# Kernel tuning notes

Hardware: AMD Instinct MI355X
Metric: run time of the kernel (lower is better)

The kernel has to match this reference:

```python
import jax, jax.numpy as jnp
import numpy as np

N_WIRES = 4
DIM = 16  # 2**4 state-vector length; wire 0 = most significant bit


def _ry(state, theta, wire):
    """Apply RY(theta) on `wire`. state: (N,16) real; theta: (N,) or scalar."""
    s = jnp.moveaxis(state.reshape(-1, 2, 2, 2, 2), 1 + wire, 1)
    c = jnp.cos(theta * 0.5)
    sn = jnp.sin(theta * 0.5)
    if jnp.ndim(theta):
        c = c.reshape(-1, 1, 1, 1)
        sn = sn.reshape(-1, 1, 1, 1)
    s0, s1 = s[:, 0], s[:, 1]
    out = jnp.stack([c * s0 - sn * s1, sn * s0 + c * s1], axis=1)
    return jnp.moveaxis(out, 1, 1 + wire).reshape(-1, DIM)


def _cx_perm(control, target):
    idx = np.arange(DIM)
    cbit = (idx >> (N_WIRES - 1 - control)) & 1
    return np.where(cbit == 1, idx ^ (1 << (N_WIRES - 1 - target)), idx)

# Pauli-Z expectation signs per wire: (16, 4)
_Z_SIGNS = np.stack(
    [1.0 - 2.0 * ((np.arange(DIM) >> (N_WIRES - 1 - w)) & 1) for w in range(N_WIRES)],
    axis=1,
).astype(np.float32)
_CX01 = _cx_perm(0, 1); _CX12 = _cx_perm(1, 2); _CX23 = _cx_perm(2, 3)
_CX02 = _cx_perm(0, 2); _CX13 = _cx_perm(1, 3)


def _init_state(n, dtype):
    return jnp.zeros((n, DIM), dtype).at[:, 0].set(1.0)  # |0000>


def _encode(angles):
    """Fresh device + RY(angle_w) on each wire. angles: (N,4) -> state (N,16)."""
    state = _init_state(angles.shape[0], angles.dtype)
    for w in range(N_WIRES):
        state = _ry(state, angles[:, w], w)
    return state


def _measure_z(state):
    return (state * state) @ jnp.asarray(_Z_SIGNS, state.dtype)  # (N,4)


def _quanv_features(angles, rl_params):
    """Encoder + fixed 8-op 'random layer' (5 RY + 3 CX) + MeasureAll(Z)."""
    s = _encode(angles)
    s = _ry(s, rl_params[0], 0)
    s = _ry(s, rl_params[1], 1)
    s = s[:, _CX02]
    s = _ry(s, rl_params[2], 2)
    s = _ry(s, rl_params[3], 3)
    s = s[:, _CX13]
    s = _ry(s, rl_params[4], 0)
    s = s[:, _CX23]
    return _measure_z(s)  # (N,4)


def _attn_raw(angles):
    """Encoder + CX(0,1),CX(1,2),CX(2,3), measure Z on wire 0."""
    s = _encode(angles)
    s = s[:, _CX01]
    s = s[:, _CX12]
    s = s[:, _CX23]
    return _measure_z(s)[:, 0]  # (N,)


def setup_inputs() -> dict:
    key = jax.random.key(0)
    k1, k2, k3 = jax.random.split(key, 3)
    B = 4096
    x = jax.random.uniform(k1, (B, 784), dtype=jnp.float32)
    rl_params = jax.random.normal(k2, (5,), dtype=jnp.float32)
    W = jax.random.normal(k3, (10, 784), dtype=jnp.float32) * 0.03
    b = jnp.zeros((10,), jnp.float32)
    return {"x": x, "rl_params": rl_params, "W": W, "b": b}


def reference(x, rl_params, W, b):
    B = x.shape[0]
    img = x.reshape(B, 28, 28)
    # 2x2 patches in row-major order -> (B*196, 4) with order [tl, tr, bl, br]
    angles = img.reshape(B, 14, 2, 14, 2).transpose(0, 1, 3, 2, 4).reshape(B * 196, 4)
    feats = _quanv_features(angles, rl_params).reshape(B, 196, 4)
    raw = _attn_raw(feats.reshape(B * 196, 4)).reshape(B, 196)
    attn = jax.nn.softmax(raw, axis=1)
    weighted = (feats * attn[:, :, None]).reshape(B, 4 * 14 * 14)
    logits = weighted @ W.T + b
    return jax.nn.log_softmax(logits, axis=-1)
```

## Files before the change

kernel.cpp:

```cpp
#include <hip/hip_runtime.h>

#define NPATCH 196


__device__ __forceinline__ float dot4(float4 a, float4 b) {
    return a.x * b.x + a.y * b.y + a.z * b.z + a.w * b.w;
}

__device__ __forceinline__ float wave_sum_bcast(float x) {
#define DPP_STEP(ctrl, rmask)                                                   \
    x += __int_as_float(__builtin_amdgcn_update_dpp(                            \
        0, __float_as_int(x), (ctrl), (rmask), 0xf, true));
    DPP_STEP(0x111, 0xf)
    DPP_STEP(0x112, 0xf)
    DPP_STEP(0x114, 0xf)
    DPP_STEP(0x118, 0xf)
    DPP_STEP(0x142, 0xa)
    DPP_STEP(0x143, 0xc)
#undef DPP_STEP
    return __int_as_float(__builtin_amdgcn_readlane(__float_as_int(x), 63));
}

__global__ __launch_bounds__(256) void quanv_fused(
    const float* __restrict__ x, const float* __restrict__ rl,
    const float* __restrict__ W, const float* __restrict__ bias,
    float* __restrict__ out)
{
    const int lane = threadIdx.x & 63;
    const int wave = threadIdx.x >> 6;
    const int img  = blockIdx.x * 4 + wave;

    const float* __restrict__ xb = x + (size_t)img * 784;

    float srl2, crl2, srl4, crl4;
    __sincosf(rl[2], &srl2, &crl2);
    __sincosf(rl[4], &srl4, &crl4);
    const float rl0 = rl[0], rl1 = rl[1], rl3v = rl[3];

    auto pairf = [&](int q, float4& fA, float4& fB, float& eA, float& eB) {
        const int r = (2 * q) / 14;
        const int c = (2 * q) - r * 14;
        const float4 top = *reinterpret_cast<const float4*>(xb + 56 * r + 2 * c);
        const float4 bot = *reinterpret_cast<const float4*>(xb + 56 * r + 2 * c + 28);
        {
            float sa, ca; __sincosf(top.x + rl0, &sa, &ca);
            float s2, c2; __sincosf(bot.x, &s2, &c2);
            const float f1 = __cosf(top.y + rl1);
            const float cd = __cosf(bot.y + rl3v);
            const float f0 = crl4 * ca - srl4 * sa * s2;
            const float f2 = crl2 * ca * c2 - srl2 * s2;
            fA = make_float4(f0, f1, f2, f1 * cd * f2);
            eA = __expf(__cosf(f0));
        }
        {
            float sa, ca; __sincosf(top.z + rl0, &sa, &ca);
            float s2, c2; __sincosf(bot.z, &s2, &c2);
            const float f1 = __cosf(top.w + rl1);
            const float cd = __cosf(bot.w + rl3v);
            const float f0 = crl4 * ca - srl4 * sa * s2;
            const float f2 = crl2 * ca * c2 - srl2 * s2;
            fB = make_float4(f0, f1, f2, f1 * cd * f2);
            eB = __expf(__cosf(f0));
        }
    };

    const bool has2 = (lane < 34);
    const int q2 = has2 ? (lane + 64) : lane;

    float4 fA0, fB0, fA1, fB1;
    float eA0, eB0, eA1, eB1;
    pairf(lane, fA0, fB0, eA0, eB0);
    pairf(q2,   fA1, fB1, eA1, eB1);
    if (!has2) { eA1 = 0.f; eB1 = 0.f; }

    const float inv = 1.0f / wave_sum_bcast(eA0 + eB0 + eA1 + eB1);

    const float wA0 = eA0 * inv, wB0 = eB0 * inv;
    const float wA1 = eA1 * inv, wB1 = eB1 * inv;
    const float4 gA0 = make_float4(fA0.x * wA0, fA0.y * wA0, fA0.z * wA0, fA0.w * wA0);
    const float4 gB0 = make_float4(fB0.x * wB0, fB0.y * wB0, fB0.z * wB0, fB0.w * wB0);
    const float4 gA1 = make_float4(fA1.x * wA1, fA1.y * wA1, fA1.z * wA1, fA1.w * wA1);
    const float4 gB1 = make_float4(fB1.x * wB1, fB1.y * wB1, fB1.z * wB1, fB1.w * wB1);

    const float4* __restrict__ W4 = reinterpret_cast<const float4*>(W);
    float acc[10];
    #pragma unroll
    for (int k = 0; k < 10; ++k) {
        const int kb = k * NPATCH;
        acc[k] = dot4(gA0, W4[kb + 2 * lane])
               + dot4(gB0, W4[kb + 2 * lane + 1])
               + dot4(gA1, W4[kb + 2 * q2])
               + dot4(gB1, W4[kb + 2 * q2 + 1]);
    }

    float lg[10];
    #pragma unroll
    for (int k = 0; k < 10; ++k) lg[k] = wave_sum_bcast(acc[k]) + bias[k];

    float m2 = lg[0];
    #pragma unroll
    for (int k = 1; k < 10; ++k) m2 = fmaxf(m2, lg[k]);
    float ssum = 0.f;
    #pragma unroll
    for (int k = 0; k < 10; ++k) ssum += __expf(lg[k] - m2);
    const float lse = m2 + __logf(ssum);

    if (lane < 10) {
        float myv = lg[0];
        #pragma unroll
        for (int k = 1; k < 10; ++k) myv = (lane == k) ? lg[k] : myv;
        out[(size_t)img * 10 + lane] = myv - lse;
    }
}

extern "C" void kernel_launch(void* const* d_in, const int* in_sizes, int n_in,
                              void* d_out, int out_size, void* d_ws, size_t ws_size,
                              hipStream_t stream) {
    const float* x    = (const float*)d_in[0];
    const float* rl   = (const float*)d_in[1];
    const float* W    = (const float*)d_in[2];
    const float* bias = (const float*)d_in[3];
    float* out = (float*)d_out;
    const int B = in_sizes[0] / 784;
    quanv_fused<<<B / 4, 256, 0, stream>>>(x, rl, W, bias, out);
}
```

Baseline: 12.18 us.

## Process four images per wave to reuse W loads across images

```diff
diff --git a/kernel.cpp b/kernel.cpp
--- a/kernel.cpp
+++ b/kernel.cpp
@@ -1,6 +1,7 @@
 #include <hip/hip_runtime.h>
 
 #define NPATCH 196
+#define IMGS 4
 
 
 __device__ __forceinline__ float dot4(float4 a, float4 b) {
@@ -21,23 +22,25 @@
     return __int_as_float(__builtin_amdgcn_readlane(__float_as_int(x), 63));
 }
 
-__global__ __launch_bounds__(256) void quanv_fused(
+__global__ __launch_bounds__(256, 1) void quanv_fused(
     const float* __restrict__ x, const float* __restrict__ rl,
     const float* __restrict__ W, const float* __restrict__ bias,
     float* __restrict__ out)
 {
     const int lane = threadIdx.x & 63;
     const int wave = threadIdx.x >> 6;
-    const int img  = blockIdx.x * 4 + wave;
-
-    const float* __restrict__ xb = x + (size_t)img * 784;
+    const int img0 = blockIdx.x * (4 * IMGS) + wave * IMGS;
 
     float srl2, crl2, srl4, crl4;
     __sincosf(rl[2], &srl2, &crl2);
     __sincosf(rl[4], &srl4, &crl4);
     const float rl0 = rl[0], rl1 = rl[1], rl3v = rl[3];
 
-    auto pairf = [&](int q, float4& fA, float4& fB, float& eA, float& eB) {
+    const bool has2 = (lane < 34);
+    const int q2 = has2 ? (lane + 64) : lane;
+
+    auto pairf = [&](const float* __restrict__ xb, int q,
+                     float4& fA, float4& fB, float& eA, float& eB) {
         const int r = (2 * q) / 14;
         const int c = (2 * q) - r * 14;
         const float4 top = *reinterpret_cast<const float4*>(xb + 56 * r + 2 * c);
@@ -64,52 +67,68 @@
         }
     };
 
-    const bool has2 = (lane < 34);
-    const int q2 = has2 ? (lane + 64) : lane;
+    float4 g[IMGS][4];
+    float  ev[IMGS][4];
+    #pragma unroll
+    for (int im = 0; im < IMGS; ++im) {
+        const float* __restrict__ xb = x + (size_t)(img0 + im) * 784;
+        pairf(xb, lane, g[im][0], g[im][1], ev[im][0], ev[im][1]);
+        pairf(xb, q2,   g[im][2], g[im][3], ev[im][2], ev[im][3]);
+        if (!has2) { ev[im][2] = 0.f; ev[im][3] = 0.f; }
+    }
 
-    float4 fA0, fB0, fA1, fB1;
-    float eA0, eB0, eA1, eB1;
-    pairf(lane, fA0, fB0, eA0, eB0);
-    pairf(q2,   fA1, fB1, eA1, eB1);
-    if (!has2) { eA1 = 0.f; eB1 = 0.f; }
-
-    const float inv = 1.0f / wave_sum_bcast(eA0 + eB0 + eA1 + eB1);
-
-    const float wA0 = eA0 * inv, wB0 = eB0 * inv;
-    const float wA1 = eA1 * inv, wB1 = eB1 * inv;
-    const float4 gA0 = make_float4(fA0.x * wA0, fA0.y * wA0, fA0.z * wA0, fA0.w * wA0);
-    const float4 gB0 = make_float4(fB0.x * wB0, fB0.y * wB0, fB0.z * wB0, fB0.w * wB0);
-    const float4 gA1 = make_float4(fA1.x * wA1, fA1.y * wA1, fA1.z * wA1, fA1.w * wA1);
-    const float4 gB1 = make_float4(fB1.x * wB1, fB1.y * wB1, fB1.z * wB1, fB1.w * wB1);
+    #pragma unroll
+    for (int im = 0; im < IMGS; ++im) {
+        const float inv = 1.0f /
+            wave_sum_bcast(ev[im][0] + ev[im][1] + ev[im][2] + ev[im][3]);
+        #pragma unroll
+        for (int j = 0; j < 4; ++j) {
+            const float w = ev[im][j] * inv;
+            g[im][j] = make_float4(g[im][j].x * w, g[im][j].y * w,
+                                   g[im][j].z * w, g[im][j].w * w);
+        }
+    }
 
     const float4* __restrict__ W4 = reinterpret_cast<const float4*>(W);
-    float acc[10];
+    float acc[IMGS][10];
     #pragma unroll
     for (int k = 0; k < 10; ++k) {
         const int kb = k * NPATCH;
-        acc[k] = dot4(gA0, W4[kb + 2 * lane])
-               + dot4(gB0, W4[kb + 2 * lane + 1])
-               + dot4(gA1, W4[kb + 2 * q2])
-               + dot4(gB1, W4[kb + 2 * q2 + 1]);
+        const float4 w0 = W4[kb + 2 * lane];
+        const float4 w1 = W4[kb + 2 * lane + 1];
+        const float4 w2 = W4[kb + 2 * q2];
+        const float4 w3 = W4[kb + 2 * q2 + 1];
+        #pragma unroll
+        for (int im = 0; im < IMGS; ++im) {
+            acc[im][k] = dot4(g[im][0], w0) + dot4(g[im][1], w1)
+                       + dot4(g[im][2], w2) + dot4(g[im][3], w3);
+        }
     }
 
-    float lg[10];
+    float lg[IMGS][10];
     #pragma unroll
-    for (int k = 0; k < 10; ++k) lg[k] = wave_sum_bcast(acc[k]) + bias[k];
+    for (int k = 0; k < 10; ++k) {
+        const float bk = bias[k];
+        #pragma unroll
+        for (int im = 0; im < IMGS; ++im)
+            lg[im][k] = wave_sum_bcast(acc[im][k]) + bk;
+    }
 
-    float m2 = lg[0];
     #pragma unroll
-    for (int k = 1; k < 10; ++k) m2 = fmaxf(m2, lg[k]);
-    float ssum = 0.f;
-    #pragma unroll
-    for (int k = 0; k < 10; ++k) ssum += __expf(lg[k] - m2);
-    const float lse = m2 + __logf(ssum);
-
-    if (lane < 10) {
-        float myv = lg[0];
+    for (int im = 0; im < IMGS; ++im) {
+        float m2 = lg[im][0];
         #pragma unroll
-        for (int k = 1; k < 10; ++k) myv = (lane == k) ? lg[k] : myv;
-        out[(size_t)img * 10 + lane] = myv - lse;
+        for (int k = 1; k < 10; ++k) m2 = fmaxf(m2, lg[im][k]);
+        float ssum = 0.f;
+        #pragma unroll
+        for (int k = 0; k < 10; ++k) ssum += __expf(lg[im][k] - m2);
+        const float lse = m2 + __logf(ssum);
+        if (lane < 10) {
+            float myv = lg[im][0];
+            #pragma unroll
+            for (int k = 1; k < 10; ++k) myv = (lane == k) ? lg[im][k] : myv;
+            out[(size_t)(img0 + im) * 10 + lane] = myv - lse;
+        }
     }
 }
 
@@ -122,5 +141,5 @@
     const float* bias = (const float*)d_in[3];
     float* out = (float*)d_out;
     const int B = in_sizes[0] / 784;
-    quanv_fused<<<B / 4, 256, 0, stream>>>(x, rl, W, bias, out);
+    quanv_fused<<<B / (4 * IMGS), 256, 0, stream>>>(x, rl, W, bias, out);
 }
```

Measured after the change: 11.98 us. Within noise of the previous version (-1.7%).
